# Optimization experiments

Measured on AMD Instinct MI355X. Metric: run time of the kernel, lower is better.

## Reference

```python
import jax, jax.numpy as jnp
import numpy as np

N = 100000
E = 1600000
D_IN = 128
D_OUT = 128


def setup_inputs() -> dict:
    key = jax.random.key(0)
    ks = jax.random.split(key, 7)
    x = jax.random.normal(ks[0], (N, D_IN), dtype=jnp.float32)
    edge_index = jax.random.randint(ks[1], (2, E), 0, N, dtype=jnp.int64)
    # parameters (PyTorch Linear init: U(-1/sqrt(fan_in), 1/sqrt(fan_in)))
    b1_bound = 1.0 / np.sqrt(D_IN)
    b2_bound = 1.0 / np.sqrt(D_OUT)
    eps = jnp.zeros((1,), dtype=jnp.float32)
    W1 = jax.random.uniform(ks[2], (D_IN, D_OUT), jnp.float32, -b1_bound, b1_bound)
    b1 = jax.random.uniform(ks[3], (D_OUT,), jnp.float32, -b1_bound, b1_bound)
    W2 = jax.random.uniform(ks[4], (D_OUT, D_OUT), jnp.float32, -b2_bound, b2_bound)
    b2 = jax.random.uniform(ks[5], (D_OUT,), jnp.float32, -b2_bound, b2_bound)
    return {"x": x, "edge_index": edge_index, "num_nodes": N,
            "eps": eps, "W1": W1, "b1": b1, "W2": W2, "b2": b2}


def reference(x, edge_index, num_nodes, eps, W1, b1, W2, b2):
    row, col = edge_index[0], edge_index[1]
    # gather source features, scatter-add into destination nodes
    agg = jax.ops.segment_sum(x[col], row, num_segments=num_nodes)  # [N, D_IN]
    h = (1.0 + eps[0]) * x + agg
    h = jax.nn.relu(h @ W1 + b1)
    out = h @ W2 + b2
    return out
```

## Files before the change

kernel.cpp:

```cpp
#include <hip/hip_runtime.h>

typedef unsigned int uint;
typedef unsigned short ushort;
typedef __attribute__((ext_vector_type(8))) short short8v;
typedef __attribute__((ext_vector_type(4))) float f32x4;
typedef __attribute__((ext_vector_type(4))) uint uint4v;

#define D 128
#define LDH 136
#define NPB 64
#define PSHIFT 26
#define NBLK 256
#define MAXNC 4096
#define SRTCAP 4096

__device__ __forceinline__ bool ei_is64(const int* ei32) {
    return ((ei32[1] | ei32[3] | ei32[5] | ei32[7]) == 0);
}
__device__ __forceinline__ float b2f(ushort u) { return __uint_as_float((uint)u << 16); }
__device__ __forceinline__ ushort f2b(float f) {
    uint a = __float_as_uint(f);
    return (ushort)((a + 0x7fffu + ((a >> 16) & 1u)) >> 16);
}
__device__ __forceinline__ uint f2b2(float lo, float hi) {
    return (uint)f2b(lo) | ((uint)f2b(hi) << 16);
}

__global__ __launch_bounds__(256) void gin_prep(
    const void* __restrict__ ei_raw, int* __restrict__ harr, int NC, int E,
    const float* __restrict__ W1, const float* __restrict__ W2,
    ushort* __restrict__ w1t, ushort* __restrict__ w2t)
{
    __shared__ int h[MAXNC];
    int bid = blockIdx.x;
    if (bid < NBLK) {
        for (int i = threadIdx.x; i < NC; i += 256) h[i] = 0;
        __syncthreads();
        const int* ei32 = (const int*)ei_raw;
        const long long* ei64 = (const long long*)ei_raw;
        const bool is64 = ei_is64(ei32);
        for (int e = bid * 256 + threadIdx.x; e < E; e += 256 * NBLK) {
            int dst = is64 ? (int)ei64[e] : ei32[e];
            atomicAdd(&h[dst >> 6], 1);
        }
        __syncthreads();
        for (int i = threadIdx.x; i < NC; i += 256)
            harr[(size_t)i * NBLK + bid] = h[i];
    } else {
        int idx = (bid - NBLK) * 256 + threadIdx.x;
        int which = idx >> 14;
        int rem   = idx & 16383;
        int k = rem & 127, n = rem >> 7;
        const float* W = which ? W2 : W1;
        ushort* WT = which ? w2t : w1t;
        WT[rem] = f2b(W[k * D + n]);
    }
}

__global__ __launch_bounds__(512) void gin_colsum(
    int* __restrict__ harr, int* __restrict__ tot, int NC)
{
    int wv   = (blockIdx.x * 512 + threadIdx.x) >> 6;
    int lane = threadIdx.x & 63;
    if (wv >= NC) return;
    int4* col = (int4*)(harr + (size_t)wv * NBLK);
    int4 v = col[lane];
    int s = v.x + v.y + v.z + v.w;
    int inc = s;
    #pragma unroll
    for (int d = 1; d < 64; d <<= 1) {
        int t = __shfl_up(inc, d, 64);
        if (lane >= d) inc += t;
    }
    int excl = inc - s;
    int4 o;
    o.x = excl; o.y = excl + v.x; o.z = o.y + v.y; o.w = o.z + v.z;
    col[lane] = o;
    if (lane == 63) tot[wv] = inc;
}

__global__ __launch_bounds__(256) void gin_cscatter(
    const void* __restrict__ ei_raw, const int* __restrict__ harr,
    const int* __restrict__ tot, int* __restrict__ coff,
    uint* __restrict__ pairs, int NC, int E,
    const float4* __restrict__ x4, uint4v* __restrict__ xb16, int n8)
{
    __shared__ int sc[MAXNC + 1];
    __shared__ int part[256];
    const int tid = threadIdx.x;
    if (blockIdx.x >= NBLK) {
        int i = (blockIdx.x - NBLK) * 256 + tid;
        if (i < n8) {
            float4 a = x4[i * 2 + 0];
            float4 b = x4[i * 2 + 1];
            uint4v o;
            o.x = f2b2(a.x, a.y); o.y = f2b2(a.z, a.w);
            o.z = f2b2(b.x, b.y); o.w = f2b2(b.z, b.w);
            xb16[i] = o;
        }
        return;
    }
    const int CH = (NC + 1 + 255) >> 8;
    const int base = tid * CH;
    int lsum = 0;
    for (int j = 0; j < CH; ++j) {
        int idx = base + j;
        if (idx < NC) lsum += tot[idx];
    }
    part[tid] = lsum;
    __syncthreads();
    for (int d = 1; d < 256; d <<= 1) {
        int t = (tid >= d) ? part[tid - d] : 0;
        __syncthreads();
        part[tid] += t;
        __syncthreads();
    }
    int run = part[tid] - lsum;
    for (int j = 0; j < CH; ++j) {
        int idx = base + j;
        if (idx <= NC) { sc[idx] = run; if (idx < NC) run += tot[idx]; }
    }
    __syncthreads();
    if (blockIdx.x == 0)
        for (int i = tid; i <= NC; i += 256) coff[i] = sc[i];
    for (int i = tid; i < NC; i += 256)
        sc[i] += harr[(size_t)i * NBLK + blockIdx.x];
    __syncthreads();
    const int* ei32 = (const int*)ei_raw;
    const long long* ei64 = (const long long*)ei_raw;
    const bool is64 = ei_is64(ei32);
    for (int e = blockIdx.x * 256 + tid; e < E; e += 256 * NBLK) {
        int dst, src;
        if (is64) { dst = (int)ei64[e]; src = (int)ei64[E + e]; }
        else      { dst = ei32[e];      src = ei32[E + e]; }
        int c = dst >> 6;
        int p = atomicAdd(&sc[c], 1);
        pairs[p] = ((uint)(dst & (NPB - 1)) << PSHIFT) | (uint)src;
    }
}

__device__ __forceinline__ void mlp8(
    ushort* S, const ushort* __restrict__ w1t, const ushort* __restrict__ w2t,
    const float* __restrict__ b1, const float* __restrict__ b2,
    float* __restrict__ out, long long n0, int N, int tid)
{
    const int w   = tid >> 6;
    const int l   = tid & 63;
    const int c16 = l & 15;
    const int g   = l >> 4;

    f32x4 acc[4];
    {
        float bv = b1[w * 16 + c16];
        #pragma unroll
        for (int m = 0; m < 4; ++m) acc[m] = (f32x4){bv, bv, bv, bv};
    }
    #pragma unroll
    for (int ks = 0; ks < 4; ++ks) {
        short8v bB = *(const short8v*)&w1t[(w * 16 + c16) * D + ks * 32 + g * 8];
        #pragma unroll
        for (int m = 0; m < 4; ++m) {
            short8v a = *(const short8v*)&S[(m * 16 + c16) * LDH + ks * 32 + g * 8];
            acc[m] = __builtin_amdgcn_mfma_f32_16x16x32_bf16(a, bB, acc[m], 0, 0, 0);
        }
    }
    __syncthreads();
    #pragma unroll
    for (int m = 0; m < 4; ++m)
        #pragma unroll
        for (int r = 0; r < 4; ++r)
            S[(m * 16 + g * 4 + r) * LDH + w * 16 + c16] = f2b(fmaxf(acc[m][r], 0.f));
    __syncthreads();
    {
        float bv = b2[w * 16 + c16];
        #pragma unroll
        for (int m = 0; m < 4; ++m) acc[m] = (f32x4){bv, bv, bv, bv};
    }
    #pragma unroll
    for (int ks = 0; ks < 4; ++ks) {
        short8v bB = *(const short8v*)&w2t[(w * 16 + c16) * D + ks * 32 + g * 8];
        #pragma unroll
        for (int m = 0; m < 4; ++m) {
            short8v a = *(const short8v*)&S[(m * 16 + c16) * LDH + ks * 32 + g * 8];
            acc[m] = __builtin_amdgcn_mfma_f32_16x16x32_bf16(a, bB, acc[m], 0, 0, 0);
        }
    }
    #pragma unroll
    for (int m = 0; m < 4; ++m)
        #pragma unroll
        for (int r = 0; r < 4; ++r) {
            long long row = n0 + m * 16 + g * 4 + r;
            if (row < N)
                __builtin_nontemporal_store(acc[m][r], &out[row * D + w * 16 + c16]);
        }
}

__global__ __launch_bounds__(512, 8) void gin_sg_mlp(
    const uint* __restrict__ pairs, const int* __restrict__ coff,
    const ushort* __restrict__ xb, const float* __restrict__ epsp,
    const ushort* __restrict__ w1t, const ushort* __restrict__ w2t,
    const float* __restrict__ b1, const float* __restrict__ b2,
    float* __restrict__ out, int N)
{
    __shared__ int4 U[(NPB * LDH * 2 + 15) / 16];
    int*    srt = (int*)U;
    ushort* S   = (ushort*)U;
    __shared__ int hist[NPB], ex[NPB], cur[NPB];
    const int c = blockIdx.x;
    const int s = coff[c], e = coff[c + 1];
    const int size = e - s;
    const int tid = threadIdx.x;
    const float epsv = 1.0f + epsp[0];
    const long long nb = (long long)c * NPB;
    const ushort4* xr = (const ushort4*)xb;
    const int lane = tid & 31, grp = tid >> 5;

    if (size <= SRTCAP) {
        if (tid < NPB) { hist[tid] = 0; cur[tid] = 0; }
        uint pr[8]; int np = 0;
        #pragma unroll
        for (int k = 0; k < 8; ++k) {
            int i = tid + k * 512;
            if (i < size) { pr[k] = __builtin_nontemporal_load(&pairs[s + i]); np = k + 1; }
        }
        __syncthreads();
        #pragma unroll
        for (int k = 0; k < 8; ++k)
            if (k < np) atomicAdd(&hist[pr[k] >> PSHIFT], 1);
        __syncthreads();
        if (tid < 64) {
            int v = hist[tid];
            int inc = v;
            #pragma unroll
            for (int d = 1; d < 64; d <<= 1) {
                int t = __shfl_up(inc, d, 64);
                if (tid >= d) inc += t;
            }
            ex[tid] = inc - v;
        }
        __syncthreads();
        #pragma unroll
        for (int k = 0; k < 8; ++k)
            if (k < np) {
                uint p = pr[k];
                int ld = p >> PSHIFT;
                int pos = atomicAdd(&cur[ld], 1);
                srt[ex[ld] + pos] = (int)(p & ((1u << PSHIFT) - 1u));
            }
        __syncthreads();
        float4 accv[4];
        #pragma unroll
        for (int q = 0; q < 4; ++q) {
            int nn = grp + q * 16;
            long long node = nb + nn;
            float4 acc = make_float4(0.f, 0.f, 0.f, 0.f);
            if (node < N) {
                ushort4 rs = xr[node * 32 + lane];
                acc.x = epsv * b2f(rs.x); acc.y = epsv * b2f(rs.y);
                acc.z = epsv * b2f(rs.z); acc.w = epsv * b2f(rs.w);
                int start = ex[nn];
                int deg   = hist[nn];
                int j = 0;
                for (; j + 8 <= deg; j += 8) {
                    int sx[8];
                    #pragma unroll
                    for (int u = 0; u < 8; ++u) sx[u] = srt[start + j + u];
                    ushort4 r[8];
                    #pragma unroll
                    for (int u = 0; u < 8; ++u) r[u] = xr[(long long)sx[u] * 32 + lane];
                    #pragma unroll
                    for (int u = 0; u < 8; ++u) {
                        acc.x += b2f(r[u].x); acc.y += b2f(r[u].y);
                        acc.z += b2f(r[u].z); acc.w += b2f(r[u].w);
                    }
                }
                for (; j < deg; ++j) {
                    int sx = srt[start + j];
                    ushort4 r = xr[(long long)sx * 32 + lane];
                    acc.x += b2f(r.x); acc.y += b2f(r.y);
                    acc.z += b2f(r.z); acc.w += b2f(r.w);
                }
            }
            accv[q] = acc;
        }
        __syncthreads();
        #pragma unroll
        for (int q = 0; q < 4; ++q) {
            int nn = grp + q * 16;
            ushort4 o;
            o.x = f2b(accv[q].x); o.y = f2b(accv[q].y);
            o.z = f2b(accv[q].z); o.w = f2b(accv[q].w);
            *(ushort4*)&S[nn * LDH + lane * 4] = o;
        }
        __syncthreads();
    } else {
        #pragma unroll
        for (int q = 0; q < 4; ++q) {
            int nn = grp + q * 16;
            long long node = nb + nn;
            float4 acc = make_float4(0.f, 0.f, 0.f, 0.f);
            if (node < N) {
                ushort4 rs = xr[node * 32 + lane];
                acc.x = epsv * b2f(rs.x); acc.y = epsv * b2f(rs.y);
                acc.z = epsv * b2f(rs.z); acc.w = epsv * b2f(rs.w);
                for (int i = 0; i < size; ++i) {
                    uint p = pairs[s + i];
                    if ((int)(p >> PSHIFT) == nn) {
                        long long sx = p & ((1u << PSHIFT) - 1u);
                        ushort4 r = xr[sx * 32 + lane];
                        acc.x += b2f(r.x); acc.y += b2f(r.y);
                        acc.z += b2f(r.z); acc.w += b2f(r.w);
                    }
                }
            }
            ushort4 o;
            o.x = f2b(acc.x); o.y = f2b(acc.y); o.z = f2b(acc.z); o.w = f2b(acc.w);
            *(ushort4*)&S[nn * LDH + lane * 4] = o;
        }
        __syncthreads();
    }
    mlp8(S, w1t, w2t, b1, b2, out, nb, N, tid);
}

extern "C" void kernel_launch(void* const* d_in, const int* in_sizes, int n_in,
                              void* d_out, int out_size, void* d_ws, size_t ws_size,
                              hipStream_t stream) {
    const float* x   = (const float*)d_in[0];
    const void*  ei  = d_in[1];
    const float* eps = (const float*)d_in[3];
    const float* W1  = (const float*)d_in[4];
    const float* b1  = (const float*)d_in[5];
    const float* W2  = (const float*)d_in[6];
    const float* b2  = (const float*)d_in[7];
    float* out = (float*)d_out;

    const int N = in_sizes[0] / D;
    const int E = in_sizes[1] / 2;
    const int NC = (N + NPB - 1) / NPB;
    const int NCp = (NC + 1 + 255) & ~255;

    int* coff   = (int*)d_ws;
    int* tot    = coff + NCp;
    int* harr   = tot + NCp;
    uint* pairs = (uint*)(harr + (size_t)NBLK * NC);
    size_t base   = ((size_t)2 * NCp + (size_t)NBLK * NC + (size_t)E) * sizeof(int);
    size_t xb_off = (base + 15) & ~(size_t)15;
    size_t w1_off = xb_off + (size_t)N * D * sizeof(ushort);
    size_t w2_off = w1_off + (size_t)D * D * sizeof(ushort);
    size_t need   = w2_off + (size_t)D * D * sizeof(ushort);

    if (ws_size < need || NC > MAXNC) return;

    ushort* xb  = (ushort*)((char*)d_ws + xb_off);
    ushort* w1t = (ushort*)((char*)d_ws + w1_off);
    ushort* w2t = (ushort*)((char*)d_ws + w2_off);

    const int n8  = N * D / 8;
    const int nxb = (n8 + 255) / 256;
    gin_prep<<<NBLK + 128, 256, 0, stream>>>(ei, harr, NC, E, W1, W2, w1t, w2t);
    gin_colsum<<<(NC * 64 + 511) / 512, 512, 0, stream>>>(harr, tot, NC);
    gin_cscatter<<<NBLK + nxb, 256, 0, stream>>>(ei, harr, tot, coff, pairs, NC, E,
                                                 (const float4*)x, (uint4v*)xb, n8);
    gin_sg_mlp<<<NC, 512, 0, stream>>>(pairs, coff, xb, eps, w1t, w2t, b1, b2, out, N);
}
```

Before: 124.7 us.

## Merge three preprocessing kernels into one cooperative kernel with grid syncs

Replaces the histogram, column-scan and counting-scatter kernels with a single cooperative kernel of 256 blocks that separates the phases with grid.sync(). The x-to-bf16 conversion and weight transpose move into this kernel, run by grid-stride loops or the first 128 blocks. The aim is to remove two kernel launches and their inter-kernel gaps. In exchange the grid is fixed at 256 blocks, so the bf16 conversion gets far less parallelism than its old dedicated blocks, and cooperative launch plus grid barriers add their own overhead.

```diff
diff --git a/kernel.cpp b/kernel.cpp
--- a/kernel.cpp
+++ b/kernel.cpp
@@ -1,4 +1,7 @@
 #include <hip/hip_runtime.h>
+#include <hip/hip_cooperative_groups.h>
+
+namespace cg = cooperative_groups;
 
 typedef unsigned int uint;
 typedef unsigned short ushort;
@@ -10,6 +13,7 @@
 #define LDH 136
 #define NPB 64
 #define PSHIFT 26
+#define SRCMASK ((1u << PSHIFT) - 1u)
 #define NBLK 256
 #define MAXNC 4096
 #define SRTCAP 4096
@@ -26,28 +30,34 @@
     return (uint)f2b(lo) | ((uint)f2b(hi) << 16);
 }
 
-__global__ __launch_bounds__(256) void gin_prep(
-    const void* __restrict__ ei_raw, int* __restrict__ harr, int NC, int E,
+__global__ __launch_bounds__(256) void gin_front(
+    const void* __restrict__ ei_raw, int* __restrict__ harr,
+    int* __restrict__ tot, int* __restrict__ coff, uint* __restrict__ pairs,
+    int NC, int E,
+    const float4* __restrict__ x4, uint4v* __restrict__ xb16, int n8,
     const float* __restrict__ W1, const float* __restrict__ W2,
     ushort* __restrict__ w1t, ushort* __restrict__ w2t)
 {
-    __shared__ int h[MAXNC];
-    int bid = blockIdx.x;
-    if (bid < NBLK) {
-        for (int i = threadIdx.x; i < NC; i += 256) h[i] = 0;
-        __syncthreads();
-        const int* ei32 = (const int*)ei_raw;
-        const long long* ei64 = (const long long*)ei_raw;
-        const bool is64 = ei_is64(ei32);
-        for (int e = bid * 256 + threadIdx.x; e < E; e += 256 * NBLK) {
-            int dst = is64 ? (int)ei64[e] : ei32[e];
-            atomicAdd(&h[dst >> 6], 1);
-        }
-        __syncthreads();
-        for (int i = threadIdx.x; i < NC; i += 256)
-            harr[(size_t)i * NBLK + bid] = h[i];
-    } else {
-        int idx = (bid - NBLK) * 256 + threadIdx.x;
+    cg::grid_group grid = cg::this_grid();
+    __shared__ int h[MAXNC + 1];
+    __shared__ int part[256];
+    const int tid = threadIdx.x;
+    const int bid = blockIdx.x;
+    const int* ei32 = (const int*)ei_raw;
+    const long long* ei64 = (const long long*)ei_raw;
+    const bool is64 = ei_is64(ei32);
+
+    for (int i = tid; i < NC; i += 256) h[i] = 0;
+    __syncthreads();
+    for (int e = bid * 256 + tid; e < E; e += 256 * NBLK) {
+        int dst = is64 ? (int)ei64[e] : ei32[e];
+        atomicAdd(&h[dst >> 6], 1);
+    }
+    __syncthreads();
+    for (int i = tid; i < NC; i += 256)
+        harr[(size_t)i * NBLK + bid] = h[i];
+    if (bid < 128) {
+        int idx = bid * 256 + tid;
         int which = idx >> 14;
         int rem   = idx & 16383;
         int k = rem & 127, n = rem >> 7;
@@ -55,87 +65,75 @@
         ushort* WT = which ? w2t : w1t;
         WT[rem] = f2b(W[k * D + n]);
     }
-}
-
-__global__ __launch_bounds__(512) void gin_colsum(
-    int* __restrict__ harr, int* __restrict__ tot, int NC)
-{
-    int wv   = (blockIdx.x * 512 + threadIdx.x) >> 6;
-    int lane = threadIdx.x & 63;
-    if (wv >= NC) return;
-    int4* col = (int4*)(harr + (size_t)wv * NBLK);
-    int4 v = col[lane];
-    int s = v.x + v.y + v.z + v.w;
-    int inc = s;
-    #pragma unroll
-    for (int d = 1; d < 64; d <<= 1) {
-        int t = __shfl_up(inc, d, 64);
-        if (lane >= d) inc += t;
-    }
-    int excl = inc - s;
-    int4 o;
-    o.x = excl; o.y = excl + v.x; o.z = o.y + v.y; o.w = o.z + v.z;
-    col[lane] = o;
-    if (lane == 63) tot[wv] = inc;
-}
-
-__global__ __launch_bounds__(256) void gin_cscatter(
-    const void* __restrict__ ei_raw, const int* __restrict__ harr,
-    const int* __restrict__ tot, int* __restrict__ coff,
-    uint* __restrict__ pairs, int NC, int E,
-    const float4* __restrict__ x4, uint4v* __restrict__ xb16, int n8)
-{
-    __shared__ int sc[MAXNC + 1];
-    __shared__ int part[256];
-    const int tid = threadIdx.x;
-    if (blockIdx.x >= NBLK) {
-        int i = (blockIdx.x - NBLK) * 256 + tid;
-        if (i < n8) {
-            float4 a = x4[i * 2 + 0];
-            float4 b = x4[i * 2 + 1];
-            uint4v o;
-            o.x = f2b2(a.x, a.y); o.y = f2b2(a.z, a.w);
-            o.z = f2b2(b.x, b.y); o.w = f2b2(b.z, b.w);
-            xb16[i] = o;
-        }
-        return;
-    }
-    const int CH = (NC + 1 + 255) >> 8;
-    const int base = tid * CH;
-    int lsum = 0;
-    for (int j = 0; j < CH; ++j) {
-        int idx = base + j;
-        if (idx < NC) lsum += tot[idx];
-    }
-    part[tid] = lsum;
-    __syncthreads();
-    for (int d = 1; d < 256; d <<= 1) {
-        int t = (tid >= d) ? part[tid - d] : 0;
-        __syncthreads();
-        part[tid] += t;
-        __syncthreads();
-    }
-    int run = part[tid] - lsum;
-    for (int j = 0; j < CH; ++j) {
-        int idx = base + j;
-        if (idx <= NC) { sc[idx] = run; if (idx < NC) run += tot[idx]; }
-    }
-    __syncthreads();
-    if (blockIdx.x == 0)
-        for (int i = tid; i <= NC; i += 256) coff[i] = sc[i];
-    for (int i = tid; i < NC; i += 256)
-        sc[i] += harr[(size_t)i * NBLK + blockIdx.x];
-    __syncthreads();
-    const int* ei32 = (const int*)ei_raw;
-    const long long* ei64 = (const long long*)ei_raw;
-    const bool is64 = ei_is64(ei32);
-    for (int e = blockIdx.x * 256 + tid; e < E; e += 256 * NBLK) {
-        int dst, src;
-        if (is64) { dst = (int)ei64[e]; src = (int)ei64[E + e]; }
-        else      { dst = ei32[e];      src = ei32[E + e]; }
-        int c = dst >> 6;
-        int p = atomicAdd(&sc[c], 1);
-        pairs[p] = ((uint)(dst & (NPB - 1)) << PSHIFT) | (uint)src;
+    __threadfence();
+    grid.sync();
+
+    {
+        int gw   = (bid * 256 + tid) >> 6;
+        int lane = tid & 63;
+        for (int col = gw; col < NC; col += 1024) {
+            int4* colp = (int4*)(harr + (size_t)col * NBLK);
+            int4 v = colp[lane];
+            int s = v.x + v.y + v.z + v.w;
+            int inc = s;
+            #pragma unroll
+            for (int d = 1; d < 64; d <<= 1) {
+                int t = __shfl_up(inc, d, 64);
+                if (lane >= d) inc += t;
+            }
+            int excl = inc - s;
+            int4 o;
+            o.x = excl; o.y = excl + v.x; o.z = o.y + v.y; o.w = o.z + v.z;
+            colp[lane] = o;
+            if (lane == 63) tot[col] = inc;
+        }
+    }
+    for (int i = bid * 256 + tid; i < n8; i += 256 * NBLK) {
+        float4 a = x4[i * 2 + 0];
+        float4 b = x4[i * 2 + 1];
+        uint4v o;
+        o.x = f2b2(a.x, a.y); o.y = f2b2(a.z, a.w);
+        o.z = f2b2(b.x, b.y); o.w = f2b2(b.z, b.w);
+        xb16[i] = o;
+    }
+    __threadfence();
+    grid.sync();
+
+    {
+        const int CH = (NC + 1 + 255) >> 8;
+        const int base = tid * CH;
+        int lsum = 0;
+        for (int j = 0; j < CH; ++j) {
+            int idx = base + j;
+            if (idx < NC) lsum += tot[idx];
+        }
+        part[tid] = lsum;
+        __syncthreads();
+        for (int d = 1; d < 256; d <<= 1) {
+            int t = (tid >= d) ? part[tid - d] : 0;
+            __syncthreads();
+            part[tid] += t;
+            __syncthreads();
+        }
+        int run = part[tid] - lsum;
+        for (int j = 0; j < CH; ++j) {
+            int idx = base + j;
+            if (idx <= NC) { h[idx] = run; if (idx < NC) run += tot[idx]; }
+        }
+        __syncthreads();
+        if (bid == 0)
+            for (int i = tid; i <= NC; i += 256) coff[i] = h[i];
+        for (int i = tid; i < NC; i += 256)
+            h[i] += harr[(size_t)i * NBLK + bid];
+        __syncthreads();
+        for (int e = bid * 256 + tid; e < E; e += 256 * NBLK) {
+            int dst, src;
+            if (is64) { dst = (int)ei64[e]; src = (int)ei64[E + e]; }
+            else      { dst = ei32[e];      src = ei32[E + e]; }
+            int c = dst >> 6;
+            int p = atomicAdd(&h[c], 1);
+            pairs[p] = ((uint)(dst & (NPB - 1)) << PSHIFT) | (uint)src;
+        }
     }
 }
 
@@ -245,7 +243,7 @@
                 uint p = pr[k];
                 int ld = p >> PSHIFT;
                 int pos = atomicAdd(&cur[ld], 1);
-                srt[ex[ld] + pos] = (int)(p & ((1u << PSHIFT) - 1u));
+                srt[ex[ld] + pos] = (int)(p & SRCMASK);
             }
         __syncthreads();
         float4 accv[4];
@@ -306,7 +304,7 @@
                 for (int i = 0; i < size; ++i) {
                     uint p = pairs[s + i];
                     if ((int)(p >> PSHIFT) == nn) {
-                        long long sx = p & ((1u << PSHIFT) - 1u);
+                        long long sx = p & SRCMASK;
                         ushort4 r = xr[sx * 32 + lane];
                         acc.x += b2f(r.x); acc.y += b2f(r.y);
                         acc.z += b2f(r.z); acc.w += b2f(r.w);
@@ -355,11 +353,18 @@
     ushort* w1t = (ushort*)((char*)d_ws + w1_off);
     ushort* w2t = (ushort*)((char*)d_ws + w2_off);
 
-    const int n8  = N * D / 8;
-    const int nxb = (n8 + 255) / 256;
-    gin_prep<<<NBLK + 128, 256, 0, stream>>>(ei, harr, NC, E, W1, W2, w1t, w2t);
-    gin_colsum<<<(NC * 64 + 511) / 512, 512, 0, stream>>>(harr, tot, NC);
-    gin_cscatter<<<NBLK + nxb, 256, 0, stream>>>(ei, harr, tot, coff, pairs, NC, E,
-                                                 (const float4*)x, (uint4v*)xb, n8);
+    int n8 = N * D / 8;
+    const float4* x4p = (const float4*)x;
+    uint4v* xb16p = (uint4v*)xb;
+    int NCv = NC, Ev = E;
+
+    void* args[] = {
+        (void*)&ei, (void*)&harr, (void*)&tot, (void*)&coff, (void*)&pairs,
+        (void*)&NCv, (void*)&Ev,
+        (void*)&x4p, (void*)&xb16p, (void*)&n8,
+        (void*)&W1, (void*)&W2, (void*)&w1t, (void*)&w2t
+    };
+    hipLaunchCooperativeKernel((void*)gin_front, dim3(NBLK), dim3(256),
+                               args, 0, stream);
     gin_sg_mlp<<<NC, 512, 0, stream>>>(pairs, coff, xb, eps, w1t, w2t, b1, b2, out, N);
 }
```

Result: slower. 261.9 us (+110.0%).
